# Kernel optimization log

Measured on AMD Instinct MI355X. Metric: run time of the kernel, lower is better.

Reference implementation:

```python
import jax, jax.numpy as jnp
import numpy as np
from jax import lax

LN_LAMBDA = 2.0  # ln_lambda from init

def setup_inputs() -> dict:
    key = jax.random.key(0)
    k1, k2, k3 = jax.random.split(key, 3)
    x = jax.random.normal(k1, (32, 32, 256, 256), dtype=jnp.float32)
    w_bar = jax.random.normal(k2, (32, 32, 3, 3), dtype=jnp.float32) * 0.1
    bias = jax.random.normal(k3, (32,), dtype=jnp.float32) * 0.1
    return {"x": x, "w_bar": w_bar, "bias": bias}

def reference(x, w_bar, bias):
    # _update_u_v: full SVD of weight reshaped to [height, -1]; torch uses
    # w.view(h,-1).data, i.e. sigma is detached from the graph.
    h = w_bar.shape[0]
    w2d = lax.stop_gradient(w_bar).reshape(h, -1)  # [32, 288]
    s = jnp.linalg.svd(w2d, full_matrices=False, compute_uv=False)
    sigma = jnp.maximum(jnp.ones_like(s[0]), s[0] / LN_LAMBDA)
    w = w_bar / sigma  # rescaled weight used by wrapped module
    # wrapped module: Conv2d(32, 32, kernel_size=3, padding=1)
    out = lax.conv_general_dilated(
        x, w,
        window_strides=(1, 1),
        padding=((1, 1), (1, 1)),
        dimension_numbers=("NCHW", "OIHW", "NCHW"),
    )
    return out + bias.reshape(1, -1, 1, 1)
```

## Files before the change

kernel.cpp:

```cpp
#include <hip/hip_runtime.h>
#include <math.h>


typedef __attribute__((ext_vector_type(8))) __bf16 frag8;
typedef __attribute__((ext_vector_type(16))) float f32x16;
typedef __attribute__((ext_vector_type(8))) unsigned short u16x8;

__device__ __forceinline__ unsigned short bf16bits(float v) {
  __bf16 h = (__bf16)v;
  return __builtin_bit_cast(unsigned short, h);
}

__global__ __launch_bounds__(256) void sn_prep_kernel(
    const float* __restrict__ w_bar,
    unsigned short* __restrict__ w_out)
{
  __shared__ __align__(16) float sw[9216];
  __shared__ __align__(16) float swT[9216];
  __shared__ float G0[1024];
  __shared__ float Gpp[2048];
  __shared__ float vvec[32];
  __shared__ float svec[32];
  __shared__ float scal[2];
  const int tid = threadIdx.x;

  for (int i = tid; i < 9216; i += 256) {
    float v = w_bar[i];
    sw[i] = v;
    int k = i / 288;
    int t = i - k * 288;
    swT[t * 32 + k] = v;
  }
  __syncthreads();

  for (int e = tid; e < 1024; e += 256) {
    int i = e >> 5, j = e & 31;
    const float* ri = &sw[i * 288];
    float s = 0.f;
    for (int t = 0; t < 288; t += 4) {
      float4 a = *(const float4*)(ri + t);
      s = fmaf(a.x, swT[(t + 0) * 32 + j], s);
      s = fmaf(a.y, swT[(t + 1) * 32 + j], s);
      s = fmaf(a.z, swT[(t + 2) * 32 + j], s);
      s = fmaf(a.w, swT[(t + 3) * 32 + j], s);
    }
    G0[e] = s;
  }

  const float* src = G0;
  for (int sq = 0; sq < 6; ++sq) {
    float* dst = &Gpp[(sq & 1) * 1024];
    __syncthreads();
    for (int e = tid; e < 1024; e += 256) {
      int i = e >> 5, j = e & 31;
      float s = 0.f;
#pragma unroll
      for (int t = 0; t < 32; ++t)
        s = fmaf(src[i * 32 + t], src[t * 32 + j], s);
      dst[e] = s;
    }
    __syncthreads();
    float s0 = dst[0];
    float inv = (s0 > 0.f) ? (1.f / s0) : 1.f;
    __syncthreads();
    for (int e = tid; e < 1024; e += 256) dst[e] *= inv;
    src = dst;
  }

  if (tid < 32) vvec[tid] = 1.f;
  __syncthreads();
  for (int it = 0; it < 4; ++it) {
    if (tid < 32) {
      float s = 0.f;
#pragma unroll
      for (int j = 0; j < 32; ++j) s = fmaf(src[tid * 32 + j], vvec[j], s);
      svec[tid] = s;
    }
    __syncthreads();
    if (tid == 0) {
      float n2 = 0.f;
      for (int j = 0; j < 32; ++j) n2 += svec[j] * svec[j];
      scal[0] = (n2 > 0.f) ? rsqrtf(n2) : 0.f;
    }
    __syncthreads();
    if (tid < 32) vvec[tid] = svec[tid] * scal[0];
    __syncthreads();
  }

  if (tid < 32) {
    float s = 0.f;
#pragma unroll
    for (int j = 0; j < 32; ++j) s = fmaf(G0[tid * 32 + j], vvec[j], s);
    svec[tid] = s * vvec[tid];
  }
  __syncthreads();
  if (tid == 0) {
    float lam = 0.f;
    for (int j = 0; j < 32; ++j) lam += svec[j];
    lam = fmaxf(lam, 0.f);
    float sigma = fmaxf(1.f, 0.5f * sqrtf(lam));
    scal[1] = 1.f / sigma;
  }
  __syncthreads();
  float inv_sigma = scal[1];
  for (int e = tid; e < 9216; e += 256) {
    int q = e >> 10;
    int rem = e & 1023;
    int k = rem >> 5;
    int c = rem & 31;
    float w = sw[k * 288 + c * 9 + q] * inv_sigma;
    __bf16 hb = (__bf16)w;
    float lo = w - (float)hb;
    w_out[e] = __builtin_bit_cast(unsigned short, hb);
    w_out[9216 + e] = bf16bits(lo);
  }
}

__global__ __launch_bounds__(256, 2) void sn_conv_mfma(
    const float* __restrict__ x, const unsigned short* __restrict__ wsp,
    const float* __restrict__ bias, float* __restrict__ out)
{
  __shared__ __align__(16) unsigned short wH[12800];
  __shared__ __align__(16) unsigned short wL[12800];
  __shared__ __align__(16) unsigned short sxH[5440];
  __shared__ __align__(16) unsigned short sxL[5440];

  const int tid  = threadIdx.x;
  const int lane = tid & 63;
  const int wv   = tid >> 6;
  const int l31  = lane & 31;
  const int half = lane >> 5;
  const int n  = blockIdx.z;
  const int y0 = blockIdx.y * 8;
  const int x0 = blockIdx.x * 64;

  {
    unsigned int* zH = (unsigned int*)wH;
    unsigned int* zL = (unsigned int*)wL;
    for (int i = tid; i < 6400; i += 256) { zH[i] = 0u; zL[i] = 0u; }
  }
  __syncthreads();
  for (int i = tid; i < 9216; i += 256) {
    int q = i >> 10, rem = i & 1023, k = rem >> 5, c = rem & 31;
    int d = (q * 32 + k) * 40 + c;
    wH[d] = wsp[i];
    wL[d] = wsp[9216 + i];
  }

  const int kb = 4 * half;
  const float4 b0 = *(const float4*)&bias[kb];
  const float4 b1 = *(const float4*)&bias[kb + 8];
  const float4 b2 = *(const float4*)&bias[kb + 16];
  const float4 b3 = *(const float4*)&bias[kb + 24];
  f32x16 acc0;
  acc0[0] = b0.x; acc0[1] = b0.y; acc0[2]  = b0.z; acc0[3]  = b0.w;
  acc0[4] = b1.x; acc0[5] = b1.y; acc0[6]  = b1.z; acc0[7]  = b1.w;
  acc0[8] = b2.x; acc0[9] = b2.y; acc0[10] = b2.z; acc0[11] = b2.w;
  acc0[12] = b3.x; acc0[13] = b3.y; acc0[14] = b3.z; acc0[15] = b3.w;
  f32x16 acc1 = acc0, acc2 = acc0, acc3 = acc0;

  int offB[5];
#pragma unroll
  for (int p = 0; p < 5; ++p) {
    int q = 2 * p + half; if (q > 8) q = 8;
    int dy = q / 3;
    int dx = q - 3 * dy;
    offB[p] = (dy * 68 + dx) * 8;
  }

  const float* xn = x + (size_t)n * 32 * 65536;

  for (int cs = 0; cs < 4; ++cs) {
    const int c0 = cs * 8;
    __syncthreads();
    for (int idx = tid; idx < 660; idx += 256) {
      int r   = idx / 66;
      int col = idx - r * 66;
      int gy = y0 - 1 + r;
      int gx = x0 - 1 + col;
      bool ok = ((unsigned)gy < 256u) && ((unsigned)gx < 256u);
      const float* px = xn + (size_t)c0 * 65536 + gy * 256 + gx;
      u16x8 hv, lv;
#pragma unroll
      for (int cl = 0; cl < 8; ++cl) {
        float v = ok ? px[(size_t)cl * 65536] : 0.f;
        __bf16 hb = (__bf16)v;
        float rl = v - (float)hb;
        hv[cl] = __builtin_bit_cast(unsigned short, hb);
        lv[cl] = bf16bits(rl);
      }
      int d = (r * 68 + col) * 8;
      *(u16x8*)&sxH[d] = hv;
      *(u16x8*)&sxL[d] = lv;
    }
    __syncthreads();

    frag8 aH[5], aL[5];
#pragma unroll
    for (int p = 0; p < 5; ++p) {
      int qa = 2 * p + half;
      int d = (qa * 32 + l31) * 40 + c0;
      aH[p] = __builtin_bit_cast(frag8, *(const u16x8*)&wH[d]);
      aL[p] = __builtin_bit_cast(frag8, *(const u16x8*)&wL[d]);
    }

#define LOAD_B(BH, BL, TT)                                                       \
    frag8 BH[5], BL[5];                                                          \
    {                                                                            \
      const int r_o = wv * 2 + ((TT) >> 1);                                      \
      const int dbase = (r_o * 68 + ((TT) & 1) * 32 + l31) * 8;                  \
      _Pragma("unroll")                                                          \
      for (int p = 0; p < 5; ++p) {                                              \
        BH[p] = __builtin_bit_cast(frag8, *(const u16x8*)&sxH[dbase + offB[p]]); \
        BL[p] = __builtin_bit_cast(frag8, *(const u16x8*)&sxL[dbase + offB[p]]); \
      }                                                                          \
    }

    {
      LOAD_B(bH0, bL0, 0)
      LOAD_B(bH1, bL1, 1)
#pragma unroll
      for (int p = 0; p < 5; ++p) {
        acc0 = __builtin_amdgcn_mfma_f32_32x32x16_bf16(aH[p], bH0[p], acc0, 0, 0, 0);
        acc1 = __builtin_amdgcn_mfma_f32_32x32x16_bf16(aH[p], bH1[p], acc1, 0, 0, 0);
        acc0 = __builtin_amdgcn_mfma_f32_32x32x16_bf16(aL[p], bH0[p], acc0, 0, 0, 0);
        acc1 = __builtin_amdgcn_mfma_f32_32x32x16_bf16(aL[p], bH1[p], acc1, 0, 0, 0);
        acc0 = __builtin_amdgcn_mfma_f32_32x32x16_bf16(aH[p], bL0[p], acc0, 0, 0, 0);
        acc1 = __builtin_amdgcn_mfma_f32_32x32x16_bf16(aH[p], bL1[p], acc1, 0, 0, 0);
      }
    }
    {
      LOAD_B(bH2, bL2, 2)
      LOAD_B(bH3, bL3, 3)
#pragma unroll
      for (int p = 0; p < 5; ++p) {
        acc2 = __builtin_amdgcn_mfma_f32_32x32x16_bf16(aH[p], bH2[p], acc2, 0, 0, 0);
        acc3 = __builtin_amdgcn_mfma_f32_32x32x16_bf16(aH[p], bH3[p], acc3, 0, 0, 0);
        acc2 = __builtin_amdgcn_mfma_f32_32x32x16_bf16(aL[p], bH2[p], acc2, 0, 0, 0);
        acc3 = __builtin_amdgcn_mfma_f32_32x32x16_bf16(aL[p], bH3[p], acc3, 0, 0, 0);
        acc2 = __builtin_amdgcn_mfma_f32_32x32x16_bf16(aH[p], bL2[p], acc2, 0, 0, 0);
        acc3 = __builtin_amdgcn_mfma_f32_32x32x16_bf16(aH[p], bL3[p], acc3, 0, 0, 0);
      }
    }
#undef LOAD_B
  }

#define ST_TILE(ACC, TT)                                                        \
  {                                                                             \
    const int r_o = wv * 2 + ((TT) >> 1);                                       \
    const int gx = x0 + ((TT) & 1) * 32 + l31;                                  \
    float* op = out + ((size_t)n * 32 + kb) * 65536 + (y0 + r_o) * 256 + gx;    \
    _Pragma("unroll")                                                           \
    for (int reg = 0; reg < 16; ++reg) {                                        \
      int krel = (reg & 3) + 8 * (reg >> 2);                                    \
      op[(size_t)krel * 65536] = ACC[reg];                                      \
    }                                                                           \
  }

  ST_TILE(acc0, 0)
  ST_TILE(acc1, 1)
  ST_TILE(acc2, 2)
  ST_TILE(acc3, 3)
#undef ST_TILE
}

extern "C" void kernel_launch(void* const* d_in, const int* in_sizes, int n_in,
                              void* d_out, int out_size, void* d_ws, size_t ws_size,
                              hipStream_t stream) {
  (void)in_sizes; (void)n_in; (void)out_size; (void)ws_size;
  const float* x     = (const float*)d_in[0];
  const float* w_bar = (const float*)d_in[1];
  const float* bias  = (const float*)d_in[2];
  float* out = (float*)d_out;
  unsigned short* wS = (unsigned short*)d_ws;

  sn_prep_kernel<<<1, 256, 0, stream>>>(w_bar, wS);
  dim3 grid(256 / 64, 256 / 8, 32);
  sn_conv_mfma<<<grid, 256, 0, stream>>>(x, wS, bias, out);
}
```

Measured before the change: 549.8 us.

## Double conv tile height to 16 rows with 512 threads and widen prep kernel

The conv kernel now processes 16 output rows per block with 512 threads, so the 18-row input halo is shared across more outputs and the per-block weight staging is amortized over twice the work. Weight staging into LDS becomes a direct vectorized copy with an unpadded 32-stride layout, replacing the zero-fill and scattered per-element writes. The single-block SVD prep kernel moves to 1024 threads, one Gram element per thread, with two accumulators per dot product. The unpadded weight layout may add LDS bank conflicts on A-fragment loads, and the bigger tile uses more LDS per block, which can lower occupancy.

```diff
diff --git a/kernel.cpp b/kernel.cpp
--- a/kernel.cpp
+++ b/kernel.cpp
@@ -11,7 +11,7 @@
   return __builtin_bit_cast(unsigned short, h);
 }
 
-__global__ __launch_bounds__(256) void sn_prep_kernel(
+__global__ __launch_bounds__(1024) void sn_prep_kernel(
     const float* __restrict__ w_bar,
     unsigned short* __restrict__ w_out)
 {
@@ -24,7 +24,7 @@
   __shared__ float scal[2];
   const int tid = threadIdx.x;
 
-  for (int i = tid; i < 9216; i += 256) {
+  for (int i = tid; i < 9216; i += 1024) {
     float v = w_bar[i];
     sw[i] = v;
     int k = i / 288;
@@ -33,37 +33,44 @@
   }
   __syncthreads();
 
-  for (int e = tid; e < 1024; e += 256) {
-    int i = e >> 5, j = e & 31;
+  {
+    const int i = tid >> 5, j = tid & 31;
     const float* ri = &sw[i * 288];
-    float s = 0.f;
-    for (int t = 0; t < 288; t += 4) {
+    float s0 = 0.f, s1 = 0.f;
+    for (int t = 0; t < 288; t += 8) {
       float4 a = *(const float4*)(ri + t);
-      s = fmaf(a.x, swT[(t + 0) * 32 + j], s);
-      s = fmaf(a.y, swT[(t + 1) * 32 + j], s);
-      s = fmaf(a.z, swT[(t + 2) * 32 + j], s);
-      s = fmaf(a.w, swT[(t + 3) * 32 + j], s);
-    }
-    G0[e] = s;
+      float4 b = *(const float4*)(ri + t + 4);
+      s0 = fmaf(a.x, swT[(t + 0) * 32 + j], s0);
+      s0 = fmaf(a.y, swT[(t + 1) * 32 + j], s0);
+      s0 = fmaf(a.z, swT[(t + 2) * 32 + j], s0);
+      s0 = fmaf(a.w, swT[(t + 3) * 32 + j], s0);
+      s1 = fmaf(b.x, swT[(t + 4) * 32 + j], s1);
+      s1 = fmaf(b.y, swT[(t + 5) * 32 + j], s1);
+      s1 = fmaf(b.z, swT[(t + 6) * 32 + j], s1);
+      s1 = fmaf(b.w, swT[(t + 7) * 32 + j], s1);
+    }
+    G0[tid] = s0 + s1;
   }
 
   const float* src = G0;
   for (int sq = 0; sq < 6; ++sq) {
     float* dst = &Gpp[(sq & 1) * 1024];
     __syncthreads();
-    for (int e = tid; e < 1024; e += 256) {
-      int i = e >> 5, j = e & 31;
-      float s = 0.f;
-#pragma unroll
-      for (int t = 0; t < 32; ++t)
-        s = fmaf(src[i * 32 + t], src[t * 32 + j], s);
-      dst[e] = s;
+    {
+      const int i = tid >> 5, j = tid & 31;
+      float s0 = 0.f, s1 = 0.f;
+#pragma unroll
+      for (int t = 0; t < 32; t += 2) {
+        s0 = fmaf(src[i * 32 + t], src[t * 32 + j], s0);
+        s1 = fmaf(src[i * 32 + t + 1], src[(t + 1) * 32 + j], s1);
+      }
+      dst[tid] = s0 + s1;
     }
     __syncthreads();
     float s0 = dst[0];
     float inv = (s0 > 0.f) ? (1.f / s0) : 1.f;
     __syncthreads();
-    for (int e = tid; e < 1024; e += 256) dst[e] *= inv;
+    dst[tid] *= inv;
     src = dst;
   }
 
@@ -103,7 +110,7 @@
   }
   __syncthreads();
   float inv_sigma = scal[1];
-  for (int e = tid; e < 9216; e += 256) {
+  for (int e = tid; e < 9216; e += 1024) {
     int q = e >> 10;
     int rem = e & 1023;
     int k = rem >> 5;
@@ -116,14 +123,14 @@
   }
 }
 
-__global__ __launch_bounds__(256, 2) void sn_conv_mfma(
+__global__ __launch_bounds__(512, 4) void sn_conv_mfma(
     const float* __restrict__ x, const unsigned short* __restrict__ wsp,
     const float* __restrict__ bias, float* __restrict__ out)
 {
-  __shared__ __align__(16) unsigned short wH[12800];
-  __shared__ __align__(16) unsigned short wL[12800];
-  __shared__ __align__(16) unsigned short sxH[5440];
-  __shared__ __align__(16) unsigned short sxL[5440];
+  __shared__ __align__(16) unsigned short wH[10240];
+  __shared__ __align__(16) unsigned short wL[10240];
+  __shared__ __align__(16) unsigned short sxH[9792];
+  __shared__ __align__(16) unsigned short sxL[9792];
 
   const int tid  = threadIdx.x;
   const int lane = tid & 63;
@@ -131,20 +138,16 @@
   const int l31  = lane & 31;
   const int half = lane >> 5;
   const int n  = blockIdx.z;
-  const int y0 = blockIdx.y * 8;
+  const int y0 = blockIdx.y * 16;
   const int x0 = blockIdx.x * 64;
 
-  {
-    unsigned int* zH = (unsigned int*)wH;
-    unsigned int* zL = (unsigned int*)wL;
-    for (int i = tid; i < 6400; i += 256) { zH[i] = 0u; zL[i] = 0u; }
-  }
-  __syncthreads();
-  for (int i = tid; i < 9216; i += 256) {
-    int q = i >> 10, rem = i & 1023, k = rem >> 5, c = rem & 31;
-    int d = (q * 32 + k) * 40 + c;
-    wH[d] = wsp[i];
-    wL[d] = wsp[9216 + i];
+  for (int i = tid; i < 1152; i += 512) {
+    ((u16x8*)wH)[i] = ((const u16x8*)wsp)[i];
+    ((u16x8*)wL)[i] = ((const u16x8*)(wsp + 9216))[i];
+  }
+  for (int i = tid; i < 1024; i += 512) {
+    wH[9216 + i] = 0;
+    wL[9216 + i] = 0;
   }
 
   const int kb = 4 * half;
@@ -173,7 +176,7 @@
   for (int cs = 0; cs < 4; ++cs) {
     const int c0 = cs * 8;
     __syncthreads();
-    for (int idx = tid; idx < 660; idx += 256) {
+    for (int idx = tid; idx < 18 * 66; idx += 512) {
       int r   = idx / 66;
       int col = idx - r * 66;
       int gy = y0 - 1 + r;
@@ -199,7 +202,7 @@
 #pragma unroll
     for (int p = 0; p < 5; ++p) {
       int qa = 2 * p + half;
-      int d = (qa * 32 + l31) * 40 + c0;
+      int d = qa * 1024 + l31 * 32 + c0;
       aH[p] = __builtin_bit_cast(frag8, *(const u16x8*)&wH[d]);
       aL[p] = __builtin_bit_cast(frag8, *(const u16x8*)&wL[d]);
     }
@@ -274,7 +277,7 @@
   float* out = (float*)d_out;
   unsigned short* wS = (unsigned short*)d_ws;
 
-  sn_prep_kernel<<<1, 256, 0, stream>>>(w_bar, wS);
-  dim3 grid(256 / 64, 256 / 8, 32);
-  sn_conv_mfma<<<grid, 256, 0, stream>>>(x, wS, bias, out);
-}
+  sn_prep_kernel<<<1, 1024, 0, stream>>>(w_bar, wS);
+  dim3 grid(256 / 64, 256 / 16, 32);
+  sn_conv_mfma<<<grid, 512, 0, stream>>>(x, wS, bias, out);
+}
```

After: 513.5 us. -6.6%, faster.
